# Kernel tuning notes

Hardware: AMD Instinct MI355X
Metric: run time of the kernel (lower is better)

Reference implementation:

```python
import jax, jax.numpy as jnp
import numpy as np

H, KVH, DH = 16, 4, 64
DIM = 1024
SCALE_BASE = 4096  # context_len
EPS = 1e-6


def rmsnorm(x, g):
    return x * jax.lax.rsqrt(jnp.mean(x * x, axis=-1, keepdims=True) + EPS) * g


def rope_tables(n, dh, dtype):
    inv_freq = 1.0 / (10000.0 ** (jnp.arange(0, dh, 2, dtype=jnp.float32) / dh))
    t = jnp.arange(n, dtype=jnp.float32) * (SCALE_BASE / n)
    freqs = t[:, None] * inv_freq[None, :]          # [n, dh/2]
    emb = jnp.concatenate([freqs, freqs], axis=-1)  # [n, dh]
    return jnp.cos(emb).astype(dtype), jnp.sin(emb).astype(dtype)


def apply_rope(x, cos, sin):
    # x: [b, h, n, dh]; cos/sin: [n, dh]
    x1, x2 = jnp.split(x, 2, axis=-1)
    rot = jnp.concatenate([-x2, x1], axis=-1)
    return x * cos + rot * sin


def setup_inputs() -> dict:
    key = jax.random.key(0)
    ks = jax.random.split(key, 12)
    B, N = 1, 2048
    std = 0.02
    inp = {
        "x": jax.random.normal(ks[0], (B, N, DIM), jnp.float32),
        "a": jax.random.normal(ks[1], (B, N, DIM), jnp.float32),
        "g_x": jnp.ones((DIM,), jnp.float32),
        "g_a": jnp.ones((DIM,), jnp.float32),
        "Wq_x": jax.random.normal(ks[2], (DIM, H * DH), jnp.float32) * std,
        "Wkv_x": jax.random.normal(ks[3], (DIM, 2 * KVH * DH), jnp.float32) * std,
        "Wq_a": jax.random.normal(ks[4], (DIM, H * DH), jnp.float32) * std,
        "Wkv_a": jax.random.normal(ks[5], (DIM, 2 * KVH * DH), jnp.float32) * std,
        "Wout_x": jax.random.normal(ks[6], (H * DH, DIM), jnp.float32) * std,
        "bout_x": jnp.zeros((DIM,), jnp.float32),
        "Wout_a": jax.random.normal(ks[7], (H * DH, DIM), jnp.float32) * std,
        "bout_a": jnp.zeros((DIM,), jnp.float32),
    }
    return inp


def _split_heads(t, h):
    b, n, hd = t.shape
    return t.reshape(b, n, h, hd // h).transpose(0, 2, 1, 3)  # b h n d


def _stream_qkv(s, g, Wq, Wkv):
    s = rmsnorm(s, g)
    q = _split_heads(s @ Wq, H)                 # [b, H, n, DH]
    kv = s @ Wkv
    k, v = jnp.split(kv, 2, axis=-1)
    k = _split_heads(k, KVH)                    # [b, KVH, n, DH]
    v = _split_heads(v, KVH)
    return q, k, v


def reference(x, a, g_x, g_a, Wq_x, Wkv_x, Wq_a, Wkv_a, Wout_x, bout_x, Wout_a, bout_a):
    B, Nx, _ = x.shape
    Na = a.shape[1]
    scale = DH ** -0.5
    r = H // KVH

    q_x, k_x, v_x = _stream_qkv(x, g_x, Wq_x, Wkv_x)
    q_a, k_a, v_a = _stream_qkv(a, g_a, Wq_a, Wkv_a)

    cos_x, sin_x = rope_tables(Nx, DH, x.dtype)
    cos_a, sin_a = rope_tables(Na, DH, a.dtype)
    q_x, k_x = apply_rope(q_x, cos_x, sin_x), apply_rope(k_x, cos_x, sin_x)
    q_a, k_a = apply_rope(q_a, cos_a, sin_a), apply_rope(k_a, cos_a, sin_a)

    # NOTE: original scales q by dim_head**-0.5 AND sdpa scales again -> 1/DH total
    q_x = q_x * scale
    q_a = q_a * scale

    # GQA expansion: einops 'b h n d -> b (r h) n d' == tile heads
    tile = lambda t: jnp.tile(t, (1, r, 1, 1))
    k_x, v_x, k_a, v_a = tile(k_x), tile(v_x), tile(k_a), tile(v_a)

    # pack [a, x] along seq
    q = jnp.concatenate([q_a, q_x], axis=2)
    k = jnp.concatenate([k_a, k_x], axis=2)
    v = jnp.concatenate([v_a, v_x], axis=2)

    scores = jnp.einsum('bhqd,bhkd->bhqk', q, k) * scale  # sdpa's own scale
    attn = jax.nn.softmax(scores, axis=-1)
    out = jnp.einsum('bhqk,bhkd->bhqd', attn, v)          # [b, H, Na+Nx, DH]

    out_a, out_x = out[:, :, :Na], out[:, :, Na:]
    merge = lambda t: t.transpose(0, 2, 1, 3).reshape(B, -1, H * DH)
    out_x = merge(out_x) @ Wout_x + bout_x
    out_a = merge(out_a) @ Wout_a + bout_a
    return out_x, out_a
```

## Files before the change

kernel.cpp:

```cpp
#include <hip/hip_runtime.h>
#include <hip/hip_bf16.h>
#include <stdint.h>
#include <math.h>


#define NSEQ 2048
#define NJ   4096
#define DIMM 1024
#define LPAD 72

typedef __attribute__((ext_vector_type(4))) float f32x4;
typedef __attribute__((ext_vector_type(8))) short bf16x8;
typedef __attribute__((ext_vector_type(4))) short bf16x4;

__device__ __forceinline__ unsigned short f2bf(float f) {
  union { float f; uint32_t u; } v; v.f = f;
  return (unsigned short)((v.u + 0x7FFFu + ((v.u >> 16) & 1u)) >> 16);
}

__device__ __forceinline__ uint32_t pack2bf(float a, float b) {
  __hip_bfloat162 h = __float22bfloat162_rn(float2{a, b});
  union { __hip_bfloat162 h; uint32_t u; } c; c.h = h;
  return c.u;
}

#if defined(__has_builtin)
#if __has_builtin(__builtin_amdgcn_exp2f)
#define FAST_EXP2(x) __builtin_amdgcn_exp2f(x)
#endif
#endif
#ifndef FAST_EXP2
#define FAST_EXP2(x) exp2f(x)
#endif

__device__ __forceinline__ void glds16(const void* g, void* l) {
  __builtin_amdgcn_global_load_lds(
      (const __attribute__((address_space(1))) unsigned int*)g,
      (__attribute__((address_space(3))) unsigned int*)l, 16, 0, 0);
}

__global__ __launch_bounds__(256) void prep_kernel(
    const float* __restrict__ xa, const float* __restrict__ xx,
    const float* __restrict__ ga, const float* __restrict__ gx,
    const float* __restrict__ wqa, const float* __restrict__ wqx,
    const float* __restrict__ wkva, const float* __restrict__ wkvx,
    const float* __restrict__ woa, const float* __restrict__ wox,
    unsigned short* __restrict__ XN, unsigned short* __restrict__ WQT,
    unsigned short* __restrict__ WKVT, unsigned short* __restrict__ WOT,
    float* __restrict__ cosT, float* __restrict__ sinT) {
  __shared__ float tile[32][33];
  __shared__ float red[4];
  int bid = blockIdx.x, t = threadIdx.x;
  if (bid < 256) {
    int idx = bid * 256 + t;
    int pos = idx >> 5, i = idx & 31;
    double inv = pow(10000.0, -(double)i / 32.0);
    double ang = (double)(2 * pos) * inv;
    cosT[idx] = (float)cos(ang);
    sinT[idx] = (float)sin(ang);
  } else if (bid < 6400) {
    int b = bid - 256;
    int z = b >> 10, yx = b & 1023;
    int n0 = (yx >> 5) * 32, k0 = (yx & 31) * 32;
    int s = z & 1, ty = z >> 1;
    int N = (ty == 1) ? 512 : 1024;
    if (n0 >= N) return;
    const float* src = (z == 0) ? wqa : (z == 1) ? wqx : (z == 2) ? wkva
                     : (z == 3) ? wkvx : (z == 4) ? woa : wox;
    unsigned short* dst = (ty == 0) ? WQT + (size_t)s * 1024 * 1024
                        : (ty == 1) ? WKVT + (size_t)s * 512 * 1024
                                    : WOT + (size_t)s * 1024 * 1024;
    int r = t >> 3, c4 = (t & 7) * 4;
    f32x4 v = *(const f32x4*)(src + (size_t)(k0 + r) * N + n0 + c4);
    tile[r][c4 + 0] = v.x; tile[r][c4 + 1] = v.y;
    tile[r][c4 + 2] = v.z; tile[r][c4 + 3] = v.w;
    __syncthreads();
    int nn = t >> 3, kk = (t & 7) * 4;
    bf16x4 o;
    o.x = (short)f2bf(tile[kk + 0][nn]);
    o.y = (short)f2bf(tile[kk + 1][nn]);
    o.z = (short)f2bf(tile[kk + 2][nn]);
    o.w = (short)f2bf(tile[kk + 3][nn]);
    *(bf16x4*)(dst + (size_t)(n0 + nn) * 1024 + k0 + kk) = o;
  } else {
    int b = bid - 6400;
    int s = b >> 11, row = b & 2047;
    const float* src = (s == 0 ? xa : xx) + (size_t)row * DIMM;
    const float* g = (s == 0 ? ga : gx);
    f32x4 v = *(const f32x4*)(src + t * 4);
    float ss = v.x * v.x + v.y * v.y + v.z * v.z + v.w * v.w;
#pragma unroll
    for (int o = 32; o > 0; o >>= 1) ss += __shfl_xor(ss, o, 64);
    if ((t & 63) == 0) red[t >> 6] = ss;
    __syncthreads();
    float tot = red[0] + red[1] + red[2] + red[3];
    float rs = rsqrtf(tot * (1.0f / DIMM) + 1e-6f);
    f32x4 gv = *(const f32x4*)(g + t * 4);
    bf16x4 o;
    o.x = (short)f2bf(v.x * rs * gv.x);
    o.y = (short)f2bf(v.y * rs * gv.y);
    o.z = (short)f2bf(v.z * rs * gv.z);
    o.w = (short)f2bf(v.w * rs * gv.w);
    *(bf16x4*)(XN + ((size_t)s * NSEQ + row) * DIMM + t * 4) = o;
  }
}

__device__ __forceinline__ void gemm128_mainloop(
    const unsigned short* __restrict__ Ag, const unsigned short* __restrict__ Bg,
    unsigned short* As, unsigned short* Bs, f32x4 acc[4][4]) {
  int t = threadIdx.x;
  int lane = t & 63, wid = t >> 6;
  int wm = (wid >> 1) * 64, wn = (wid & 1) * 64;
  int l15 = lane & 15, quad = lane >> 4;
  int srow = t >> 2, sko = (t & 3) * 8;
  const unsigned short* ga = Ag + (size_t)srow * 1024 + sko;
  const unsigned short* gb = Bg + (size_t)srow * 1024 + sko;
  unsigned short* la = As + t * 8;
  unsigned short* lb = Bs + t * 8;
#pragma unroll
  for (int mi = 0; mi < 4; ++mi)
#pragma unroll
    for (int j = 0; j < 4; ++j) acc[mi][j] = (f32x4){0.f, 0.f, 0.f, 0.f};
  for (int kt = 0; kt < 32; ++kt) {
    int k0 = kt * 32;
    __syncthreads();
    glds16(ga + k0, la);
    glds16(ga + 64 * 1024 + k0, la + 2048);
    glds16(gb + k0, lb);
    glds16(gb + 64 * 1024 + k0, lb + 2048);
    __syncthreads();
    bf16x8 af[4], bfr[4];
#pragma unroll
    for (int mi = 0; mi < 4; ++mi)
      af[mi] = *(const bf16x8*)(As + (wm + mi * 16 + l15) * 32 + quad * 8);
#pragma unroll
    for (int j = 0; j < 4; ++j)
      bfr[j] = *(const bf16x8*)(Bs + (wn + j * 16 + l15) * 32 + quad * 8);
#pragma unroll
    for (int mi = 0; mi < 4; ++mi)
#pragma unroll
      for (int j = 0; j < 4; ++j)
        acc[mi][j] = __builtin_amdgcn_mfma_f32_16x16x32_bf16(af[mi], bfr[j],
                                                             acc[mi][j], 0, 0, 0);
  }
}

__global__ __launch_bounds__(256) void gemm_qkv_kernel(
    const unsigned short* __restrict__ XN, const unsigned short* __restrict__ WQT,
    const unsigned short* __restrict__ WKVT, const float* __restrict__ cosT,
    const float* __restrict__ sinT, unsigned short* __restrict__ QB,
    unsigned short* __restrict__ KB, unsigned short* __restrict__ VT) {
  __shared__ unsigned short As[128 * 32], Bs[128 * 32];
  int n0 = blockIdx.x * 128, m0 = blockIdx.y * 128;
  int s = (m0 >= 2048) ? 1 : 0;
  const unsigned short* Ag = XN + (size_t)m0 * 1024;
  const unsigned short* Bg = (n0 < 1024)
      ? WQT + (size_t)s * 1024 * 1024 + (size_t)n0 * 1024
      : WKVT + (size_t)s * 512 * 1024 + (size_t)(n0 - 1024) * 1024;
  f32x4 acc[4][4];
  gemm128_mainloop(Ag, Bg, As, Bs, acc);
  int t = threadIdx.x, lane = t & 63, wid = t >> 6;
  int wm = (wid >> 1) * 64, wn = (wid & 1) * 64;
  int l15 = lane & 15, quad = lane >> 4;
  int coln = n0 + wn;
  if (coln < 1280) {
    bool isq = coln < 1024;
    float sc = isq ? (1.4426950408889634f / 64.0f) : 1.0f;
    unsigned short* dstBase;
    if (isq) dstBase = QB + (size_t)(coln >> 6) * NJ * 64;
    else     dstBase = KB + (size_t)((coln - 1024) >> 6) * NJ * 64;
#pragma unroll
    for (int mi = 0; mi < 4; ++mi)
#pragma unroll
      for (int r = 0; r < 4; ++r) {
        int jr = m0 + wm + mi * 16 + quad * 4 + r;
        int pos = jr & 2047;
#pragma unroll
        for (int jp = 0; jp < 2; ++jp) {
          int i = jp * 16 + l15;
          float c = cosT[pos * 32 + i], sn = sinT[pos * 32 + i];
          float x1 = acc[mi][jp][r], x2 = acc[mi][jp + 2][r];
          dstBase[(size_t)jr * 64 + jp * 16 + l15]      = f2bf((x1 * c - x2 * sn) * sc);
          dstBase[(size_t)jr * 64 + 32 + jp * 16 + l15] = f2bf((x2 * c + x1 * sn) * sc);
        }
      }
  } else {
    int cvb = coln - 1280;
#pragma unroll
    for (int mi = 0; mi < 4; ++mi)
#pragma unroll
      for (int j = 0; j < 4; ++j) {
        int d = cvb + j * 16 + l15;
        int jr0 = m0 + wm + mi * 16 + quad * 4;
        union { bf16x4 v; uint32_t u[2]; } pv;
        pv.u[0] = pack2bf(acc[mi][j][0], acc[mi][j][1]);
        pv.u[1] = pack2bf(acc[mi][j][2], acc[mi][j][3]);
        *(bf16x4*)(VT + (size_t)d * NJ + jr0) = pv.v;
      }
  }
}

__global__ __launch_bounds__(256, 4) void attn_kernel(
    const unsigned short* __restrict__ QB, const unsigned short* __restrict__ KB,
    const unsigned short* __restrict__ VT, unsigned short* __restrict__ AT) {
  __shared__ unsigned short Ks[2][64 * LPAD];
  __shared__ unsigned short Vs[2][64 * LPAD];
  int h = blockIdx.y, qt = blockIdx.x;
  int hk = h & 3;
  int t = threadIdx.x, lane = t & 63, w = t >> 6;
  int l15 = lane & 15, quad = lane >> 4;
  int q0 = qt * 128 + w * 16;
  bf16x8 qf[2][2];
#pragma unroll
  for (int mi = 0; mi < 2; ++mi) {
    const unsigned short* qp = QB + ((size_t)h * NJ + q0 + mi * 64 + l15) * 64;
    qf[mi][0] = *(const bf16x8*)(qp + quad * 8);
    qf[mi][1] = *(const bf16x8*)(qp + 32 + quad * 8);
  }
  f32x4 oT[2][4];
  f32x4 oL[2];
#pragma unroll
  for (int mi = 0; mi < 2; ++mi) {
    oL[mi] = (f32x4){0.f, 0.f, 0.f, 0.f};
#pragma unroll
    for (int db = 0; db < 4; ++db) oT[mi][db] = (f32x4){0.f, 0.f, 0.f, 0.f};
  }
  bf16x8 vone;
  {
    short one = (l15 == 0) ? (short)0x3F80 : (short)0;
    vone = (bf16x8){one, one, one, one, one, one, one, one};
  }
  const unsigned short* Kg = KB + (size_t)hk * NJ * 64;
  const unsigned short* Vg = VT + (size_t)hk * 64 * NJ;
  int ky = t >> 3, dof = (t & 7) * 8;
  int pky = (ky & 0x23) | ((ky & 0x18) >> 1) | ((ky & 0x04) << 2);
  const unsigned short* KgA = Kg + (size_t)ky * 64 + dof;
  const unsigned short* KgB = Kg + (size_t)(32 + ky) * 64 + dof;
  const unsigned short* VgA = Vg + (size_t)ky * NJ + dof;
  const unsigned short* VgB = Vg + (size_t)(32 + ky) * NJ + dof;
  bf16x8 kr0 = *(const bf16x8*)(KgA);
  bf16x8 kr1 = *(const bf16x8*)(KgB);
  bf16x8 vr0 = *(const bf16x8*)(VgA);
  bf16x8 vr1 = *(const bf16x8*)(VgB);
  *(bf16x8*)(Ks[0] + pky * LPAD + dof) = kr0;
  *(bf16x8*)(Ks[0] + (32 + pky) * LPAD + dof) = kr1;
  *(bf16x8*)(Vs[0] + ky * LPAD + dof) = vr0;
  *(bf16x8*)(Vs[0] + (32 + ky) * LPAD + dof) = vr1;
  kr0 = *(const bf16x8*)(KgA + 4096);
  kr1 = *(const bf16x8*)(KgB + 4096);
  vr0 = *(const bf16x8*)(VgA + 64);
  vr1 = *(const bf16x8*)(VgB + 64);
  __syncthreads();
  for (int kt = 0; kt < 64; ++kt) {
    int cur = kt & 1;
    unsigned short* Kd = Ks[cur ^ 1];
    unsigned short* Vd = Vs[cur ^ 1];
    *(bf16x8*)(Kd + pky * LPAD + dof) = kr0;
    *(bf16x8*)(Kd + (32 + pky) * LPAD + dof) = kr1;
    *(bf16x8*)(Vd + ky * LPAD + dof) = vr0;
    *(bf16x8*)(Vd + (32 + ky) * LPAD + dof) = vr1;
    int tn = (kt + 2) & 63;
    kr0 = *(const bf16x8*)(KgA + (size_t)tn * 4096);
    kr1 = *(const bf16x8*)(KgB + (size_t)tn * 4096);
    vr0 = *(const bf16x8*)(VgA + tn * 64);
    vr1 = *(const bf16x8*)(VgB + tn * 64);
    const unsigned short* Kc = Ks[cur];
    const unsigned short* Vc = Vs[cur];
    f32x4 sx[2][4];
#pragma unroll
    for (int jb = 0; jb < 4; ++jb) {
      const unsigned short* kp = Kc + (jb * 16 + l15) * LPAD;
      bf16x8 kf0 = *(const bf16x8*)(kp + quad * 8);
      bf16x8 kf1 = *(const bf16x8*)(kp + 32 + quad * 8);
      f32x4 z0 = (f32x4){0.f, 0.f, 0.f, 0.f};
      z0 = __builtin_amdgcn_mfma_f32_16x16x32_bf16(kf0, qf[0][0], z0, 0, 0, 0);
      z0 = __builtin_amdgcn_mfma_f32_16x16x32_bf16(kf1, qf[0][1], z0, 0, 0, 0);
      sx[0][jb] = z0;
      f32x4 z1 = (f32x4){0.f, 0.f, 0.f, 0.f};
      z1 = __builtin_amdgcn_mfma_f32_16x16x32_bf16(kf0, qf[1][0], z1, 0, 0, 0);
      z1 = __builtin_amdgcn_mfma_f32_16x16x32_bf16(kf1, qf[1][1], z1, 0, 0, 0);
      sx[1][jb] = z1;
    }
    bf16x8 pb[2][2];
#pragma unroll
    for (int mi = 0; mi < 2; ++mi)
#pragma unroll
      for (int sb = 0; sb < 2; ++sb) {
        union { bf16x8 v; uint32_t u[4]; } pk;
        pk.u[0] = pack2bf(FAST_EXP2(sx[mi][2 * sb][0]), FAST_EXP2(sx[mi][2 * sb][1]));
        pk.u[1] = pack2bf(FAST_EXP2(sx[mi][2 * sb][2]), FAST_EXP2(sx[mi][2 * sb][3]));
        pk.u[2] = pack2bf(FAST_EXP2(sx[mi][2 * sb + 1][0]), FAST_EXP2(sx[mi][2 * sb + 1][1]));
        pk.u[3] = pack2bf(FAST_EXP2(sx[mi][2 * sb + 1][2]), FAST_EXP2(sx[mi][2 * sb + 1][3]));
        pb[mi][sb] = pk.v;
      }
#pragma unroll
    for (int db = 0; db < 4; ++db)
#pragma unroll
      for (int sb = 0; sb < 2; ++sb) {
        bf16x8 va = *(const bf16x8*)(Vc + (db * 16 + l15) * LPAD + sb * 32 + quad * 8);
        oT[0][db] = __builtin_amdgcn_mfma_f32_16x16x32_bf16(va, pb[0][sb],
                                                            oT[0][db], 0, 0, 0);
        oT[1][db] = __builtin_amdgcn_mfma_f32_16x16x32_bf16(va, pb[1][sb],
                                                            oT[1][db], 0, 0, 0);
      }
#pragma unroll
    for (int mi = 0; mi < 2; ++mi)
#pragma unroll
      for (int sb = 0; sb < 2; ++sb)
        oL[mi] = __builtin_amdgcn_mfma_f32_16x16x32_bf16(vone, pb[mi][sb],
                                                         oL[mi], 0, 0, 0);
    __syncthreads();
  }
#pragma unroll
  for (int mi = 0; mi < 2; ++mi) {
    float s = oL[mi][0];
    s += __shfl_xor(s, 16, 64);
    s += __shfl_xor(s, 32, 64);
    float inv = 1.0f / s;
    int qrow = q0 + mi * 64 + l15;
#pragma unroll
    for (int db = 0; db < 4; ++db) {
      union { bf16x4 v; uint32_t u[2]; } ov;
      ov.u[0] = pack2bf(oT[mi][db][0] * inv, oT[mi][db][1] * inv);
      ov.u[1] = pack2bf(oT[mi][db][2] * inv, oT[mi][db][3] * inv);
      *(bf16x4*)(AT + (size_t)qrow * DIMM + h * 64 + db * 16 + quad * 4) = ov.v;
    }
  }
}

__global__ __launch_bounds__(256) void gemm_out_kernel(
    const unsigned short* __restrict__ AT, const unsigned short* __restrict__ WOT,
    const float* __restrict__ ba, const float* __restrict__ bx,
    float* __restrict__ out) {
  __shared__ unsigned short As[128 * 32], Bs[128 * 32];
  int n0 = blockIdx.x * 128, m0 = blockIdx.y * 128;
  int s = (m0 >= 2048) ? 1 : 0;
  const unsigned short* Ag = AT + (size_t)m0 * 1024;
  const unsigned short* Bg = WOT + (size_t)s * 1024 * 1024 + (size_t)n0 * 1024;
  f32x4 acc[4][4];
  gemm128_mainloop(Ag, Bg, As, Bs, acc);
  int t = threadIdx.x, lane = t & 63, wid = t >> 6;
  int wm = (wid >> 1) * 64, wn = (wid & 1) * 64;
  int l15 = lane & 15, quad = lane >> 4;
  const float* bias = s ? bx : ba;
  float* obase = s ? (out + (size_t)(m0 - 2048) * 1024)
                   : (out + (size_t)2048 * 1024 + (size_t)m0 * 1024);
#pragma unroll
  for (int mi = 0; mi < 4; ++mi)
#pragma unroll
    for (int r = 0; r < 4; ++r) {
      int row = wm + mi * 16 + quad * 4 + r;
#pragma unroll
      for (int j = 0; j < 4; ++j) {
        int col = n0 + wn + j * 16 + l15;
        obase[(size_t)row * 1024 + col] = acc[mi][j][r] + bias[col];
      }
    }
}

extern "C" void kernel_launch(void* const* d_in, const int* in_sizes, int n_in,
                              void* d_out, int out_size, void* d_ws, size_t ws_size,
                              hipStream_t stream) {
  const float* x      = (const float*)d_in[0];
  const float* a      = (const float*)d_in[1];
  const float* g_x    = (const float*)d_in[2];
  const float* g_a    = (const float*)d_in[3];
  const float* Wq_x   = (const float*)d_in[4];
  const float* Wkv_x  = (const float*)d_in[5];
  const float* Wq_a   = (const float*)d_in[6];
  const float* Wkv_a  = (const float*)d_in[7];
  const float* Wout_x = (const float*)d_in[8];
  const float* bout_x = (const float*)d_in[9];
  const float* Wout_a = (const float*)d_in[10];
  const float* bout_a = (const float*)d_in[11];
  float* out = (float*)d_out;

  char* ws = (char*)d_ws;
  const size_t MB = 1024 * 1024;
  unsigned short* XN   = (unsigned short*)(ws);
  unsigned short* WQT  = (unsigned short*)(ws + 8 * MB);
  unsigned short* WKVT = (unsigned short*)(ws + 12 * MB);
  unsigned short* WOT  = (unsigned short*)(ws + 14 * MB);
  unsigned short* QB   = (unsigned short*)(ws + 18 * MB);
  unsigned short* KB   = (unsigned short*)(ws + 26 * MB);
  unsigned short* VT   = (unsigned short*)(ws + 28 * MB);
  float* cosT          = (float*)(ws + 30 * MB);
  float* sinT          = (float*)(ws + 30 * MB + 262144);
  unsigned short* AT   = XN;

  prep_kernel<<<dim3(10496), dim3(256), 0, stream>>>(
      a, x, g_a, g_x, Wq_a, Wq_x, Wkv_a, Wkv_x, Wout_a, Wout_x,
      XN, WQT, WKVT, WOT, cosT, sinT);
  gemm_qkv_kernel<<<dim3(12, 32), dim3(256), 0, stream>>>(
      XN, WQT, WKVT, cosT, sinT, QB, KB, VT);
  attn_kernel<<<dim3(32, 16), dim3(256), 0, stream>>>(QB, KB, VT, AT);
  gemm_out_kernel<<<dim3(8, 32), dim3(256), 0, stream>>>(
      AT, WOT, bout_a, bout_x, out);
}
```

Baseline: 232.3 us.

## Split attention over two key halves and merge partials inside output GEMM

The attention grid gains a z dimension so that each block processes half of the 4096 keys. This doubles the block count from 512 to 1024 to improve CU occupancy and load balance. Each block writes unnormalized bf16 partial outputs and per-row softmax denominators. The output projection GEMM now loads both partials, sums them, divides by the combined denominator and writes the result to LDS before the MFMA. The merge appears correct only because the softmax uses no running max (scores are small), and it adds extra partial-output traffic plus a non-async A-load path in the GEMM.

```diff
diff --git a/kernel.cpp b/kernel.cpp
--- a/kernel.cpp
+++ b/kernel.cpp
@@ -37,6 +37,24 @@
   __builtin_amdgcn_global_load_lds(
       (const __attribute__((address_space(1))) unsigned int*)g,
       (__attribute__((address_space(3))) unsigned int*)l, 16, 0, 0);
+}
+
+__device__ __forceinline__ void combine8(const unsigned short* a,
+                                         const unsigned short* b, float inv,
+                                         unsigned short* dst) {
+  union { bf16x8 v; uint32_t u[4]; } ua, ub, uo;
+  ua.v = *(const bf16x8*)a;
+  ub.v = *(const bf16x8*)b;
+#pragma unroll
+  for (int i = 0; i < 4; ++i) {
+    union { uint32_t u; float f; } lo1, lo2, hi1, hi2;
+    lo1.u = ua.u[i] << 16;
+    lo2.u = ub.u[i] << 16;
+    hi1.u = ua.u[i] & 0xFFFF0000u;
+    hi2.u = ub.u[i] & 0xFFFF0000u;
+    uo.u[i] = pack2bf((lo1.f + lo2.f) * inv, (hi1.f + hi2.f) * inv);
+  }
+  *(bf16x8*)dst = uo.v;
 }
 
 __global__ __launch_bounds__(256) void prep_kernel(
@@ -202,10 +220,11 @@
 
 __global__ __launch_bounds__(256, 4) void attn_kernel(
     const unsigned short* __restrict__ QB, const unsigned short* __restrict__ KB,
-    const unsigned short* __restrict__ VT, unsigned short* __restrict__ AT) {
+    const unsigned short* __restrict__ VT, unsigned short* __restrict__ OP,
+    float* __restrict__ LS) {
   __shared__ unsigned short Ks[2][64 * LPAD];
   __shared__ unsigned short Vs[2][64 * LPAD];
-  int h = blockIdx.y, qt = blockIdx.x;
+  int h = blockIdx.y, qt = blockIdx.x, z = blockIdx.z;
   int hk = h & 3;
   int t = threadIdx.x, lane = t & 63, w = t >> 6;
   int l15 = lane & 15, quad = lane >> 4;
@@ -230,8 +249,8 @@
     short one = (l15 == 0) ? (short)0x3F80 : (short)0;
     vone = (bf16x8){one, one, one, one, one, one, one, one};
   }
-  const unsigned short* Kg = KB + (size_t)hk * NJ * 64;
-  const unsigned short* Vg = VT + (size_t)hk * 64 * NJ;
+  const unsigned short* Kg = KB + ((size_t)hk * NJ + (size_t)z * 2048) * 64;
+  const unsigned short* Vg = VT + (size_t)hk * 64 * NJ + z * 2048;
   int ky = t >> 3, dof = (t & 7) * 8;
   int pky = (ky & 0x23) | ((ky & 0x18) >> 1) | ((ky & 0x04) << 2);
   const unsigned short* KgA = Kg + (size_t)ky * 64 + dof;
@@ -251,7 +270,7 @@
   vr0 = *(const bf16x8*)(VgA + 64);
   vr1 = *(const bf16x8*)(VgB + 64);
   __syncthreads();
-  for (int kt = 0; kt < 64; ++kt) {
+  for (int kt = 0; kt < 32; ++kt) {
     int cur = kt & 1;
     unsigned short* Kd = Ks[cur ^ 1];
     unsigned short* Vd = Vs[cur ^ 1];
@@ -259,7 +278,7 @@
     *(bf16x8*)(Kd + (32 + pky) * LPAD + dof) = kr1;
     *(bf16x8*)(Vd + ky * LPAD + dof) = vr0;
     *(bf16x8*)(Vd + (32 + ky) * LPAD + dof) = vr1;
-    int tn = (kt + 2) & 63;
+    int tn = (kt + 2) & 31;
     kr0 = *(const bf16x8*)(KgA + (size_t)tn * 4096);
     kr1 = *(const bf16x8*)(KgB + (size_t)tn * 4096);
     vr0 = *(const bf16x8*)(VgA + tn * 64);
@@ -316,32 +335,70 @@
     float s = oL[mi][0];
     s += __shfl_xor(s, 16, 64);
     s += __shfl_xor(s, 32, 64);
-    float inv = 1.0f / s;
     int qrow = q0 + mi * 64 + l15;
+    if (quad == 0) LS[(size_t)(z * NJ + qrow) * 16 + h] = s;
 #pragma unroll
     for (int db = 0; db < 4; ++db) {
       union { bf16x4 v; uint32_t u[2]; } ov;
-      ov.u[0] = pack2bf(oT[mi][db][0] * inv, oT[mi][db][1] * inv);
-      ov.u[1] = pack2bf(oT[mi][db][2] * inv, oT[mi][db][3] * inv);
-      *(bf16x4*)(AT + (size_t)qrow * DIMM + h * 64 + db * 16 + quad * 4) = ov.v;
+      ov.u[0] = pack2bf(oT[mi][db][0], oT[mi][db][1]);
+      ov.u[1] = pack2bf(oT[mi][db][2], oT[mi][db][3]);
+      *(bf16x4*)(OP + ((size_t)z * NJ + qrow) * DIMM + h * 64 + db * 16 + quad * 4) = ov.v;
     }
   }
 }
 
 __global__ __launch_bounds__(256) void gemm_out_kernel(
-    const unsigned short* __restrict__ AT, const unsigned short* __restrict__ WOT,
+    const unsigned short* __restrict__ OP, const float* __restrict__ LS,
+    const unsigned short* __restrict__ WOT,
     const float* __restrict__ ba, const float* __restrict__ bx,
     float* __restrict__ out) {
   __shared__ unsigned short As[128 * 32], Bs[128 * 32];
   int n0 = blockIdx.x * 128, m0 = blockIdx.y * 128;
   int s = (m0 >= 2048) ? 1 : 0;
-  const unsigned short* Ag = AT + (size_t)m0 * 1024;
   const unsigned short* Bg = WOT + (size_t)s * 1024 * 1024 + (size_t)n0 * 1024;
-  f32x4 acc[4][4];
-  gemm128_mainloop(Ag, Bg, As, Bs, acc);
   int t = threadIdx.x, lane = t & 63, wid = t >> 6;
   int wm = (wid >> 1) * 64, wn = (wid & 1) * 64;
   int l15 = lane & 15, quad = lane >> 4;
+  int srow = t >> 2, sko = (t & 3) * 8;
+  int q = m0 + srow;
+  const unsigned short* op0 = OP + (size_t)q * DIMM + sko;
+  const unsigned short* op1 = OP + (size_t)(NJ + q) * DIMM + sko;
+  const float* ls0 = LS + (size_t)q * 16;
+  const float* ls1 = LS + (size_t)(NJ + q) * 16;
+  const unsigned short* gb = Bg + (size_t)srow * 1024 + sko;
+  unsigned short* la = As + t * 8;
+  unsigned short* lb = Bs + t * 8;
+  f32x4 acc[4][4];
+#pragma unroll
+  for (int mi = 0; mi < 4; ++mi)
+#pragma unroll
+    for (int j = 0; j < 4; ++j) acc[mi][j] = (f32x4){0.f, 0.f, 0.f, 0.f};
+  for (int kt = 0; kt < 32; ++kt) {
+    int k0 = kt * 32;
+    int hh = (k0 + sko) >> 6;
+    __syncthreads();
+    float inva = 1.0f / (ls0[hh] + ls1[hh]);
+    float invb = 1.0f / (ls0[64 * 16 + hh] + ls1[64 * 16 + hh]);
+    combine8(op0 + k0, op1 + k0, inva, la);
+    combine8(op0 + (size_t)64 * DIMM + k0, op1 + (size_t)64 * DIMM + k0, invb,
+             la + 2048);
+    glds16(gb + k0, lb);
+    glds16(gb + 64 * 1024 + k0, lb + 2048);
+    __syncthreads();
+    bf16x8 af[4], bfr[4];
+#pragma unroll
+    for (int mi = 0; mi < 4; ++mi)
+      af[mi] = *(const bf16x8*)(As + (wm + mi * 16 + l15) * 32 + quad * 8);
+#pragma unroll
+    for (int j = 0; j < 4; ++j)
+      bfr[j] = *(const bf16x8*)(Bs + (wn + j * 16 + l15) * 32 + quad * 8);
+#pragma unroll
+    for (int mi = 0; mi < 4; ++mi)
+#pragma unroll
+      for (int j = 0; j < 4; ++j)
+        acc[mi][j] = __builtin_amdgcn_mfma_f32_16x16x32_bf16(af[mi], bfr[j],
+                                                             acc[mi][j], 0, 0, 0);
+  }
   const float* bias = s ? bx : ba;
   float* obase = s ? (out + (size_t)(m0 - 2048) * 1024)
                    : (out + (size_t)2048 * 1024 + (size_t)m0 * 1024);
@@ -377,23 +434,24 @@
 
   char* ws = (char*)d_ws;
   const size_t MB = 1024 * 1024;
+  unsigned short* OP   = (unsigned short*)(ws);
   unsigned short* XN   = (unsigned short*)(ws);
   unsigned short* WQT  = (unsigned short*)(ws + 8 * MB);
   unsigned short* WKVT = (unsigned short*)(ws + 12 * MB);
-  unsigned short* WOT  = (unsigned short*)(ws + 14 * MB);
-  unsigned short* QB   = (unsigned short*)(ws + 18 * MB);
-  unsigned short* KB   = (unsigned short*)(ws + 26 * MB);
-  unsigned short* VT   = (unsigned short*)(ws + 28 * MB);
-  float* cosT          = (float*)(ws + 30 * MB);
-  float* sinT          = (float*)(ws + 30 * MB + 262144);
-  unsigned short* AT   = XN;
+  unsigned short* WOT  = (unsigned short*)(ws + 16 * MB);
+  unsigned short* QB   = (unsigned short*)(ws + 20 * MB);
+  unsigned short* KB   = (unsigned short*)(ws + 28 * MB);
+  unsigned short* VT   = (unsigned short*)(ws + 30 * MB);
+  float* cosT          = (float*)(ws + 32 * MB);
+  float* sinT          = (float*)(ws + 32 * MB + 262144);
+  float* LS            = (float*)(ws + 33 * MB);
 
   prep_kernel<<<dim3(10496), dim3(256), 0, stream>>>(
       a, x, g_a, g_x, Wq_a, Wq_x, Wkv_a, Wkv_x, Wout_a, Wout_x,
       XN, WQT, WKVT, WOT, cosT, sinT);
   gemm_qkv_kernel<<<dim3(12, 32), dim3(256), 0, stream>>>(
       XN, WQT, WKVT, cosT, sinT, QB, KB, VT);
-  attn_kernel<<<dim3(32, 16), dim3(256), 0, stream>>>(QB, KB, VT, AT);
+  attn_kernel<<<dim3(32, 16, 2), dim3(256), 0, stream>>>(QB, KB, VT, OP, LS);
   gemm_out_kernel<<<dim3(8, 32), dim3(256), 0, stream>>>(
-      AT, WOT, bout_a, bout_x, out);
-}
+      OP, LS, WOT, bout_a, bout_x, out);
+}
```

New measurement: 246.6 us. 1.06x slower.
